# Kernel optimization log

Measured on AMD Instinct MI355X. Metric: run time of the kernel, lower is better.

The kernel has to match this reference:

```python
import jax, jax.numpy as jnp
import numpy as np

B, C, H, W = 8, 256, 64, 64
OUT, K = 256, 3
OG = 1
STRIDE, PAD, DIL = 1, 1, 1
K2 = K * K


def setup_inputs() -> dict:
    key = jax.random.key(0)
    ks = jax.random.split(key, 5)
    x = jax.random.normal(ks[0], (B, C, H, W), jnp.float32)
    # main deform-conv weight [out, in//groups, k, k]
    weight = jax.random.normal(ks[1], (OUT, C, K, K), jnp.float32) * (1.0 / np.sqrt(C * K2))
    bias = jax.random.normal(ks[2], (OUT,), jnp.float32) * 0.01
    # param_generator: 3x3 conv -> 3*OG*K*K channels (oh, ow, mask)
    pg_w = jax.random.normal(ks[3], (3 * OG * K2, C, 3, 3), jnp.float32) * 0.01
    pg_b = jax.random.normal(ks[4], (3 * OG * K2,), jnp.float32) * 0.01
    return {"x": x, "weight": weight, "bias": bias, "pg_w": pg_w, "pg_b": pg_b}


def _conv3x3(x, w, b):
    y = jax.lax.conv_general_dilated(
        x, w, (1, 1), [(1, 1), (1, 1)],
        dimension_numbers=("NCHW", "OIHW", "NCHW"))
    return y + b[None, :, None, None]


def _bilinear_gather(img, py, px):
    # img [B,C,H,W]; py,px [B,K2,Ho,Wo] -> [B,C,K2,Ho,Wo]
    # Zero padding outside the image (torchvision deform_conv2d semantics).
    Hh, Ww = img.shape[2], img.shape[3]
    y0 = jnp.floor(py)
    x0 = jnp.floor(px)
    dy = py - y0
    dx = px - x0
    imgf = img.reshape(img.shape[0], img.shape[1], Hh * Ww)
    out = jnp.zeros((img.shape[0], img.shape[1]) + py.shape[1:], img.dtype)
    corners = (
        (0, 0, (1 - dy) * (1 - dx)),
        (0, 1, (1 - dy) * dx),
        (1, 0, dy * (1 - dx)),
        (1, 1, dy * dx),
    )
    for oy, ox, wgt in corners:
        yy = y0 + oy
        xx = x0 + ox
        valid = (yy >= 0) & (yy < Hh) & (xx >= 0) & (xx < Ww)
        yi = jnp.clip(yy, 0, Hh - 1).astype(jnp.int32)
        xi = jnp.clip(xx, 0, Ww - 1).astype(jnp.int32)
        idx = yi * Ww + xi  # [B,K2,Ho,Wo]
        g = jax.vmap(lambda im, ix: jnp.take(im, ix.reshape(-1), axis=1))(imgf, idx)
        g = g.reshape(img.shape[0], img.shape[1], *idx.shape[1:])
        out = out + g * (wgt * valid)[:, None]
    return out


def _deform_conv2d(x, weight, bias, pg_w, pg_b):
    Bn = x.shape[0]
    Hi, Wi = x.shape[2], x.shape[3]
    Ho = (Hi + 2 * PAD - DIL * (K - 1) - 1) // STRIDE + 1
    Wo = (Wi + 2 * PAD - DIL * (K - 1) - 1) // STRIDE + 1
    params = _conv3x3(x, pg_w, pg_b)  # [B, 3*OG*K2, H, W]
    oh, ow, mask = jnp.split(params, 3, axis=1)
    offset = jnp.concatenate([oh, ow], axis=1)  # [B, 2*OG*K2, Ho, Wo]
    mask = jax.nn.sigmoid(mask)                  # [B, OG*K2, Ho, Wo]
    # torchvision layout: channel = ((og*K2 + k)*2 + {y,x})
    off = offset.reshape(Bn, OG, K2, 2, Ho, Wo)
    dy = off[:, :, :, 0].reshape(Bn, K2, Ho, Wo)  # OG == 1
    dx = off[:, :, :, 1].reshape(Bn, K2, Ho, Wo)
    hy = jnp.arange(Ho, dtype=x.dtype) * STRIDE - PAD
    wx = jnp.arange(Wo, dtype=x.dtype) * STRIDE - PAD
    ky, kx = jnp.meshgrid(jnp.arange(K), jnp.arange(K), indexing="ij")
    base_y = hy[None, :, None] + (ky.reshape(-1) * DIL).astype(x.dtype)[:, None, None]  # [K2,Ho,1]
    base_x = wx[None, None, :] + (kx.reshape(-1) * DIL).astype(x.dtype)[:, None, None]  # [K2,1,Wo]
    py = dy + base_y[None]  # [B,K2,Ho,Wo]
    px = dx + base_x[None]
    sampled = _bilinear_gather(x, py, px)          # [B,C,K2,Ho,Wo]
    sampled = sampled * mask[:, None]              # modulation (OG=1)
    out = jnp.einsum("bckhw,ock->bohw", sampled, weight.reshape(OUT, C, K2))
    return out + bias[None, :, None, None]


def reference(x, weight, bias, pg_w, pg_b):
    return _deform_conv2d(x, weight, bias, pg_w, pg_b)
```

## Files before the change

kernel.cpp:

```cpp
#include <hip/hip_runtime.h>
#include <math.h>

#define BQ   8
#define CIN  256
#define HH   64
#define WW   64
#define COUT 256
#define K2   9
#define PCH  27

#define PT     64
#define CCH    32
#define NCHUNK (CIN / CCH)
#define NSTEP  72
#define NSUB   24
#define SUBROW 104
#define PLANE  (HH * WW)

#define NXT    (BQ * HH * 4)
#define NPW    ((NSTEP * COUT * 4) / 256)
#define NPG    ((NSTEP * 32 * 4) / 256)
#define NPREP  (NXT + NPW + NPG)

typedef __attribute__((ext_vector_type(8))) short short8;
typedef __attribute__((ext_vector_type(4))) float f32x4;
typedef __attribute__((ext_vector_type(2))) float f32x2;

#define PIPE_BARRIER() do {                                   \
    asm volatile("s_waitcnt lgkmcnt(0)" ::: "memory");        \
    __builtin_amdgcn_s_barrier();                             \
    asm volatile("" ::: "memory");                            \
} while (0)

static __device__ __forceinline__ unsigned short f2bf(float f) {
    unsigned u = __builtin_bit_cast(unsigned, f);
    u += 0x7fff + ((u >> 16) & 1);
    return (unsigned short)(u >> 16);
}
static __device__ __forceinline__ f32x2 up2(unsigned u) {
    f32x2 r;
    r[0] = __builtin_bit_cast(float, u << 16);
    r[1] = __builtin_bit_cast(float, u & 0xffff0000u);
    return r;
}
static __device__ __forceinline__ unsigned cvtpk(float lo, float hi) {
    unsigned r;
    asm("v_cvt_pk_bf16_f32 %0, %1, %2" : "=v"(r) : "v"(lo), "v"(hi));
    return r;
}

__global__ __launch_bounds__(256) void k_prep(const float* __restrict__ x,
                                              unsigned short* __restrict__ xT,
                                              const float* __restrict__ w,
                                              unsigned short* __restrict__ wp,
                                              const float* __restrict__ pgw,
                                              unsigned short* __restrict__ wpg) {
    __shared__ float tile[64][65];
    int blk = blockIdx.x;

    if (blk < NXT) {
        int cc  = blk & 3;
        int y   = (blk >> 2) & 63;
        int b   = blk >> 8;
        int t   = threadIdx.x;
        int c0  = cc * 64;

        const float* xp = x + ((size_t)(b * CIN + c0) * HH + y) * WW;
#pragma unroll
        for (int r = 0; r < 16; ++r) {
            int cl = r * 4 + (t >> 6);
            int xx = t & 63;
            tile[cl][xx] = xp[(size_t)cl * PLANE + xx];
        }
        __syncthreads();
        unsigned short* op = xT + ((size_t)b * PLANE + (size_t)y * WW) * CIN + c0;
#pragma unroll
        for (int r = 0; r < 16; ++r) {
            int xx = r * 4 + (t >> 6);
            int cl = t & 63;
            op[(size_t)xx * CIN + cl] = f2bf(tile[cl][xx]);
        }
    } else if (blk < NXT + NPW) {
        int t = (blk - NXT) * 256 + threadIdx.x;
        int q = t & 3;
        int o = (t >> 2) & 255;
        int s = t >> 10;
        short8 sv;
#pragma unroll
        for (int j = 0; j < 8; ++j) {
            int pos   = s * 32 + q * 8 + j;
            int chunk = pos / (CCH * K2);
            int pl    = pos % (CCH * K2);
            int ktap  = pl >> 5;
            int c     = chunk * CCH + (pl & 31);
            sv[j] = (short)f2bf(w[(o * CIN + c) * K2 + ktap]);
        }
        *(short8*)(wp + (size_t)t * 8) = sv;
    } else {
        int t = (blk - NXT - NPW) * 256 + threadIdx.x;
        int q = t & 3;
        int o = (t >> 2) & 31;
        int s = t >> 7;
        short8 sv;
#pragma unroll
        for (int j = 0; j < 8; ++j) {
            int pos   = s * 32 + q * 8 + j;
            int chunk = pos / (CCH * K2);
            int pl    = pos % (CCH * K2);
            int ktap  = pl >> 5;
            int c     = chunk * CCH + (pl & 31);
            sv[j] = (o < PCH) ? (short)f2bf(pgw[(size_t)(o * CIN + c) * K2 + ktap]) : (short)0;
        }
        *(short8*)(wpg + (size_t)t * 8) = sv;
    }
}

__global__ __launch_bounds__(512, 2) void k_params(const unsigned short* __restrict__ xT,
                                                   const unsigned short* __restrict__ wpg,
                                                   const float* __restrict__ pgb,
                                                   float* __restrict__ pv) {
    __shared__ alignas(16) unsigned short s_rows[2][4][66][40];

    int blk = blockIdx.x;
    int swz = (blk & 7) * 32 + (blk >> 3);
    int b   = swz >> 5;
    int h0  = (swz & 31) * 2;
    int t   = threadIdx.x;

    int wv  = t >> 6;
    int lm  = t & 15;
    int lq  = (t >> 4) & 3;
    int ipg = wv >> 2;
    int seg = wv & 3;
    int ryb = seg >> 1;
    int pxb = (seg & 1) * 32;

    const unsigned short* xTb = xT + (size_t)b * PLANE * CIN;

    if (t < 64) {
        int buf = t >> 5;
        int ry  = (t >> 3) & 3;
        int col = ((t >> 2) & 1) * 65;
        int q   = t & 3;
        uint4 z = make_uint4(0, 0, 0, 0);
        *(uint4*)&s_rows[buf][ry][col][q * 8] = z;
    }
    __syncthreads();

    f32x4 acc0 = (f32x4){0.f, 0.f, 0.f, 0.f};
    f32x4 acc1 = (f32x4){0.f, 0.f, 0.f, 0.f};

    int pxm1 = t >> 3;
    int cgs  = (t & 7) * 4;

    uint2 R[4];
#pragma unroll
    for (int ry = 0; ry < 4; ++ry) {
        int y = h0 + ry - 1;
        R[ry] = make_uint2(0, 0);
        if ((unsigned)y < (unsigned)HH)
            R[ry] = *(const uint2*)(xTb + (size_t)(y * WW + pxm1) * CIN + cgs);
    }

    for (int ch = 0; ch < NCHUNK; ++ch) {
#pragma unroll
        for (int ry = 0; ry < 4; ++ry)
            *(uint2*)&s_rows[ch & 1][ry][pxm1 + 1][cgs] = R[ry];
        if (ch + 1 < NCHUNK) {
#pragma unroll
            for (int ry = 0; ry < 4; ++ry) {
                int y = h0 + ry - 1;
                R[ry] = make_uint2(0, 0);
                if ((unsigned)y < (unsigned)HH)
                    R[ry] = *(const uint2*)(xTb + (size_t)(y * WW + pxm1) * CIN
                                            + (ch + 1) * CCH + cgs);
            }
        }
        __syncthreads();
#pragma unroll
        for (int tap = 0; tap < K2; ++tap) {
            int ky = tap / 3, kx = tap % 3;
            short8 a  = *(const short8*)(wpg + (size_t)(ch * K2 + tap) * 32 * 32
                                         + (ipg * 16 + lm) * 32 + lq * 8);
            short8 bf0 = *(const short8*)&s_rows[ch & 1][ryb + ky][pxb +  0 + lm + kx][lq * 8];
            short8 bf1 = *(const short8*)&s_rows[ch & 1][ryb + ky][pxb + 16 + lm + kx][lq * 8];
            acc0 = __builtin_amdgcn_mfma_f32_16x16x32_bf16(a, bf0, acc0, 0, 0, 0);
            acc1 = __builtin_amdgcn_mfma_f32_16x16x32_bf16(a, bf1, acc1, 0, 0, 0);
        }
    }

    float* pvo = pv + ((size_t)(b * PCH) << 12) + (h0 + ryb) * WW;
#pragma unroll
    for (int rg = 0; rg < 4; ++rg) {
        int oc = ipg * 16 + lq * 4 + rg;
        if (oc < PCH) {
            float bb = pgb[oc];
            pvo[((size_t)oc << 12) + pxb +  0 + lm] = acc0[rg] + bb;
            pvo[((size_t)oc << 12) + pxb + 16 + lm] = acc1[rg] + bb;
        }
    }
}

__global__ __launch_bounds__(512, 4) void k_fused(const unsigned short* __restrict__ xT,
                                                  const unsigned short* __restrict__ wp,
                                                  const float* __restrict__ pv,
                                                  const float* __restrict__ bias,
                                                  float* __restrict__ out) {
    __shared__ alignas(16) unsigned short s_samp[2][PT][SUBROW];
    __shared__ float4 s_wgt4[K2][PT];
    __shared__ int4   s_off4[K2][PT];

    int blk = blockIdx.x;
    int swz = (blk & 7) * 64 + (blk >> 3);
    int b   = swz >> 6;
    int h   = swz & 63;
    int t   = threadIdx.x;

    int gp = t >> 3;
    int cg = t & 7;
    int wv = t >> 6;
    int lm = t & 15;
    int lq = (t >> 4) & 3;

    const char* xTb = (const char*)xT + (size_t)b * PLANE * CIN * 2;

    const float* pvb = pv + ((size_t)(b * PCH) << 12) + h * WW;
    for (int e = t; e < K2 * PT; e += 512) {
        int k = e >> 6;
        int p = e & 63;
        float dy = pvb[(size_t)(2 * k) << 12 | (unsigned)p];
        float dx = pvb[(size_t)(2 * k + 1) << 12 | (unsigned)p];
        float mz = pvb[(size_t)(18 + k) << 12 | (unsigned)p];
        float m  = 1.f / (1.f + expf(-mz));

        float py = dy + (float)(h - 1 + k / 3);
        float px = dx + (float)(p - 1 + k % 3);
        float y0f = floorf(py), x0f = floorf(px);
        float fy = py - y0f,    fx = px - x0f;
        int iy0 = (int)y0f, ix0 = (int)x0f;
        int iy1 = iy0 + 1,  ix1 = ix0 + 1;
        bool vy0 = (unsigned)iy0 < (unsigned)HH;
        bool vy1 = (unsigned)iy1 < (unsigned)HH;
        bool vx0 = (unsigned)ix0 < (unsigned)WW;
        bool vx1 = (unsigned)ix1 < (unsigned)WW;

        float w00 = (1.f - fy) * (1.f - fx) * m; if (!(vy0 && vx0)) w00 = 0.f;
        float w01 = (1.f - fy) * fx         * m; if (!(vy0 && vx1)) w01 = 0.f;
        float w10 = fy         * (1.f - fx) * m; if (!(vy1 && vx0)) w10 = 0.f;
        float w11 = fy         * fx         * m; if (!(vy1 && vx1)) w11 = 0.f;

        int cy0 = min(max(iy0, 0), HH - 1), cy1 = min(max(iy1, 0), HH - 1);
        int cx0 = min(max(ix0, 0), WW - 1), cx1 = min(max(ix1, 0), WW - 1);

        s_wgt4[k][p] = make_float4(w00, w01, w10, w11);
        s_off4[k][p] = make_int4((cy0 * WW + cx0) * 512, (cy0 * WW + cx1) * 512,
                                 (cy1 * WW + cx0) * 512, (cy1 * WW + cx1) * 512);
    }
    __syncthreads();

    int ow = wv * 32;
    f32x4 acc[2][4];
#pragma unroll
    for (int i = 0; i < 2; ++i)
#pragma unroll
        for (int j = 0; j < 4; ++j) acc[i][j] = (f32x4){0.f, 0.f, 0.f, 0.f};

    uint2 G[3][4];
    {
#pragma unroll
        for (int j = 0; j < 3; ++j) {
            int4 ob = s_off4[j][gp];
            G[j][0] = *(const uint2*)(xTb + ob.x + cg * 8);
            G[j][1] = *(const uint2*)(xTb + ob.y + cg * 8);
            G[j][2] = *(const uint2*)(xTb + ob.z + cg * 8);
            G[j][3] = *(const uint2*)(xTb + ob.w + cg * 8);
        }
#pragma unroll
        for (int j = 0; j < 3; ++j) {
            float4 gw = s_wgt4[j][gp];
            f32x2 v01 = gw.x * up2(G[j][0].x) + gw.y * up2(G[j][1].x)
                      + gw.z * up2(G[j][2].x) + gw.w * up2(G[j][3].x);
            f32x2 v23 = gw.x * up2(G[j][0].y) + gw.y * up2(G[j][1].y)
                      + gw.z * up2(G[j][2].y) + gw.w * up2(G[j][3].y);
            uint2 pk;
            pk.x = cvtpk(v01[0], v01[1]);
            pk.y = cvtpk(v23[0], v23[1]);
            *(uint2*)&s_samp[0][gp][j * 32 + cg * 4] = pk;
        }
#pragma unroll
        for (int j = 0; j < 3; ++j) {
            int4 ob = s_off4[3 + j][gp];
            G[j][0] = *(const uint2*)(xTb + ob.x + cg * 8);
            G[j][1] = *(const uint2*)(xTb + ob.y + cg * 8);
            G[j][2] = *(const uint2*)(xTb + ob.z + cg * 8);
            G[j][3] = *(const uint2*)(xTb + ob.w + cg * 8);
        }
        PIPE_BARRIER();
    }

    short8 a0c = *(const short8*)(wp + (ow +  0 + lm) * 32 + lq * 8);
    short8 a1c = *(const short8*)(wp + (ow + 16 + lm) * 32 + lq * 8);
    for (int sc = 0; sc < NSUB; ++sc) {
        bool doC = (sc + 1 < NSUB);
        bool doL = (sc + 2 < NSUB);
        int t1 = ((sc + 1) % 3) * 3;
        int t2 = ((sc + 2) % 3) * 3;
        int c2 = ((sc + 2) / 3) * (CCH * 2) + cg * 8;
        unsigned short (*__restrict__ bc)[SUBROW] = s_samp[sc & 1];
        unsigned short (*__restrict__ bn)[SUBROW] = s_samp[(sc + 1) & 1];
#pragma unroll
        for (int sl = 0; sl < 3; ++sl) {
            short8 b0 = *(const short8*)&bc[ 0 + lm][sl * 32 + lq * 8];
            short8 b1 = *(const short8*)&bc[16 + lm][sl * 32 + lq * 8];
            short8 b2 = *(const short8*)&bc[32 + lm][sl * 32 + lq * 8];
            short8 b3 = *(const short8*)&bc[48 + lm][sl * 32 + lq * 8];
            int r = sc * 3 + sl + 1;
            short8 a0n = a0c, a1n = a1c;
            if (r < NSTEP) {
                const unsigned short* wrn = wp + (size_t)r * COUT * 32;
                a0n = *(const short8*)(wrn + (ow +  0 + lm) * 32 + lq * 8);
                a1n = *(const short8*)(wrn + (ow + 16 + lm) * 32 + lq * 8);
            }
            if (doC) {
                float4 gw = s_wgt4[t1 + sl][gp];
                f32x2 v01 = gw.x * up2(G[sl][0].x) + gw.y * up2(G[sl][1].x)
                          + gw.z * up2(G[sl][2].x) + gw.w * up2(G[sl][3].x);
                f32x2 v23 = gw.x * up2(G[sl][0].y) + gw.y * up2(G[sl][1].y)
                          + gw.z * up2(G[sl][2].y) + gw.w * up2(G[sl][3].y);
                uint2 pk;
                pk.x = cvtpk(v01[0], v01[1]);
                pk.y = cvtpk(v23[0], v23[1]);
                *(uint2*)&bn[gp][sl * 32 + cg * 4] = pk;
            }
            if (doL) {
                int4 ob = s_off4[t2 + sl][gp];
                G[sl][0] = *(const uint2*)(xTb + ob.x + c2);
                G[sl][1] = *(const uint2*)(xTb + ob.y + c2);
                G[sl][2] = *(const uint2*)(xTb + ob.z + c2);
                G[sl][3] = *(const uint2*)(xTb + ob.w + c2);
            }
            acc[0][0] = __builtin_amdgcn_mfma_f32_16x16x32_bf16(a0c, b0, acc[0][0], 0, 0, 0);
            acc[0][1] = __builtin_amdgcn_mfma_f32_16x16x32_bf16(a0c, b1, acc[0][1], 0, 0, 0);
            acc[0][2] = __builtin_amdgcn_mfma_f32_16x16x32_bf16(a0c, b2, acc[0][2], 0, 0, 0);
            acc[0][3] = __builtin_amdgcn_mfma_f32_16x16x32_bf16(a0c, b3, acc[0][3], 0, 0, 0);
            acc[1][0] = __builtin_amdgcn_mfma_f32_16x16x32_bf16(a1c, b0, acc[1][0], 0, 0, 0);
            acc[1][1] = __builtin_amdgcn_mfma_f32_16x16x32_bf16(a1c, b1, acc[1][1], 0, 0, 0);
            acc[1][2] = __builtin_amdgcn_mfma_f32_16x16x32_bf16(a1c, b2, acc[1][2], 0, 0, 0);
            acc[1][3] = __builtin_amdgcn_mfma_f32_16x16x32_bf16(a1c, b3, acc[1][3], 0, 0, 0);
            a0c = a0n; a1c = a1n;
        }
        PIPE_BARRIER();
    }

    float* op = out + ((size_t)b * COUT) * PLANE + h * WW;
#pragma unroll
    for (int i = 0; i < 2; ++i) {
        int o0 = ow + i * 16 + lq * 4;
        f32x4 bv = *(const f32x4*)(bias + o0);
#pragma unroll
        for (int rg = 0; rg < 4; ++rg) {
#pragma unroll
            for (int j = 0; j < 4; ++j)
                op[(size_t)(o0 + rg) * PLANE + j * 16 + lm] = acc[i][j][rg] + bv[rg];
        }
    }
}

extern "C" void kernel_launch(void* const* d_in, const int* in_sizes, int n_in,
                              void* d_out, int out_size, void* d_ws, size_t ws_size,
                              hipStream_t stream) {
    const float* x    = (const float*)d_in[0];
    const float* wgt  = (const float*)d_in[1];
    const float* bias = (const float*)d_in[2];
    const float* pgw  = (const float*)d_in[3];
    const float* pgb  = (const float*)d_in[4];
    float* out = (float*)d_out;

    const size_t WPK_B = (size_t)NSTEP * COUT * 32 * 2;
    const size_t WPG_B = (size_t)NSTEP * 32 * 32 * 2;
    const size_t XT_B  = (size_t)BQ * PLANE * CIN * 2;
    unsigned short* wpk = (unsigned short*)d_ws;
    unsigned short* wpg = (unsigned short*)((char*)d_ws + WPK_B);
    unsigned short* xT  = (unsigned short*)((char*)d_ws + WPK_B + WPG_B);
    float*          pv  = (float*)((char*)d_ws + WPK_B + WPG_B + XT_B);

    k_prep  <<<NPREP, 256, 0, stream>>>(x, xT, wgt, wpk, pgw, wpg);
    k_params<<<BQ * HH / 2, 512, 0, stream>>>(xT, wpg, pgb, pv);
    k_fused <<<BQ * HH, 512, 0, stream>>>(xT, wpk, pv, bias, out);
}
```

Measured before the change: 104.3 us.

## Split fused deform-conv block into producer and consumer wave groups

```diff
diff --git a/kernel.cpp b/kernel.cpp
--- a/kernel.cpp
+++ b/kernel.cpp
@@ -216,8 +216,6 @@
     int h   = swz & 63;
     int t   = threadIdx.x;
 
-    int gp = t >> 3;
-    int cg = t & 7;
     int wv = t >> 6;
     int lm = t & 15;
     int lq = (t >> 4) & 3;
@@ -258,22 +256,28 @@
     }
     __syncthreads();
 
-    int ow = wv * 32;
-    f32x4 acc[2][4];
-#pragma unroll
-    for (int i = 0; i < 2; ++i)
+    bool producer = (wv < 4);
+    int gp = t >> 2;
+    int cq = t & 3;
+    int ow = (wv - 4) * 64;
+
+    f32x4 acc[4][4];
+#pragma unroll
+    for (int i = 0; i < 4; ++i)
 #pragma unroll
         for (int j = 0; j < 4; ++j) acc[i][j] = (f32x4){0.f, 0.f, 0.f, 0.f};
 
-    uint2 G[3][4];
-    {
+    uint4 G[3][4];
+    short8 aC[4], aN[4];
+
+    if (producer) {
 #pragma unroll
         for (int j = 0; j < 3; ++j) {
             int4 ob = s_off4[j][gp];
-            G[j][0] = *(const uint2*)(xTb + ob.x + cg * 8);
-            G[j][1] = *(const uint2*)(xTb + ob.y + cg * 8);
-            G[j][2] = *(const uint2*)(xTb + ob.z + cg * 8);
-            G[j][3] = *(const uint2*)(xTb + ob.w + cg * 8);
+            G[j][0] = *(const uint4*)(xTb + ob.x + cq * 16);
+            G[j][1] = *(const uint4*)(xTb + ob.y + cq * 16);
+            G[j][2] = *(const uint4*)(xTb + ob.z + cq * 16);
+            G[j][3] = *(const uint4*)(xTb + ob.w + cq * 16);
         }
 #pragma unroll
         for (int j = 0; j < 3; ++j) {
@@ -282,86 +286,119 @@
                       + gw.z * up2(G[j][2].x) + gw.w * up2(G[j][3].x);
             f32x2 v23 = gw.x * up2(G[j][0].y) + gw.y * up2(G[j][1].y)
                       + gw.z * up2(G[j][2].y) + gw.w * up2(G[j][3].y);
-            uint2 pk;
+            f32x2 v45 = gw.x * up2(G[j][0].z) + gw.y * up2(G[j][1].z)
+                      + gw.z * up2(G[j][2].z) + gw.w * up2(G[j][3].z);
+            f32x2 v67 = gw.x * up2(G[j][0].w) + gw.y * up2(G[j][1].w)
+                      + gw.z * up2(G[j][2].w) + gw.w * up2(G[j][3].w);
+            uint4 pk;
             pk.x = cvtpk(v01[0], v01[1]);
             pk.y = cvtpk(v23[0], v23[1]);
-            *(uint2*)&s_samp[0][gp][j * 32 + cg * 4] = pk;
+            pk.z = cvtpk(v45[0], v45[1]);
+            pk.w = cvtpk(v67[0], v67[1]);
+            *(uint4*)&s_samp[0][gp][j * 32 + cq * 8] = pk;
         }
 #pragma unroll
         for (int j = 0; j < 3; ++j) {
             int4 ob = s_off4[3 + j][gp];
-            G[j][0] = *(const uint2*)(xTb + ob.x + cg * 8);
-            G[j][1] = *(const uint2*)(xTb + ob.y + cg * 8);
-            G[j][2] = *(const uint2*)(xTb + ob.z + cg * 8);
-            G[j][3] = *(const uint2*)(xTb + ob.w + cg * 8);
-        }
-        PIPE_BARRIER();
-    }
-
-    short8 a0c = *(const short8*)(wp + (ow +  0 + lm) * 32 + lq * 8);
-    short8 a1c = *(const short8*)(wp + (ow + 16 + lm) * 32 + lq * 8);
+            G[j][0] = *(const uint4*)(xTb + ob.x + cq * 16);
+            G[j][1] = *(const uint4*)(xTb + ob.y + cq * 16);
+            G[j][2] = *(const uint4*)(xTb + ob.z + cq * 16);
+            G[j][3] = *(const uint4*)(xTb + ob.w + cq * 16);
+        }
+    } else {
+#pragma unroll
+        for (int i = 0; i < 4; ++i)
+            aC[i] = *(const short8*)(wp + (ow + i * 16 + lm) * 32 + lq * 8);
+    }
+    PIPE_BARRIER();
+
     for (int sc = 0; sc < NSUB; ++sc) {
-        bool doC = (sc + 1 < NSUB);
-        bool doL = (sc + 2 < NSUB);
-        int t1 = ((sc + 1) % 3) * 3;
-        int t2 = ((sc + 2) % 3) * 3;
-        int c2 = ((sc + 2) / 3) * (CCH * 2) + cg * 8;
         unsigned short (*__restrict__ bc)[SUBROW] = s_samp[sc & 1];
         unsigned short (*__restrict__ bn)[SUBROW] = s_samp[(sc + 1) & 1];
-#pragma unroll
-        for (int sl = 0; sl < 3; ++sl) {
-            short8 b0 = *(const short8*)&bc[ 0 + lm][sl * 32 + lq * 8];
-            short8 b1 = *(const short8*)&bc[16 + lm][sl * 32 + lq * 8];
-            short8 b2 = *(const short8*)&bc[32 + lm][sl * 32 + lq * 8];
-            short8 b3 = *(const short8*)&bc[48 + lm][sl * 32 + lq * 8];
-            int r = sc * 3 + sl + 1;
-            short8 a0n = a0c, a1n = a1c;
-            if (r < NSTEP) {
-                const unsigned short* wrn = wp + (size_t)r * COUT * 32;
-                a0n = *(const short8*)(wrn + (ow +  0 + lm) * 32 + lq * 8);
-                a1n = *(const short8*)(wrn + (ow + 16 + lm) * 32 + lq * 8);
+        if (producer) {
+            bool doC = (sc + 1 < NSUB);
+            bool doL = (sc + 2 < NSUB);
+            int t1 = ((sc + 1) % 3) * 3;
+            int t2 = ((sc + 2) % 3) * 3;
+            int c2 = ((sc + 2) / 3) * (CCH * 2) + cq * 16;
+#pragma unroll
+            for (int sl = 0; sl < 3; ++sl) {
+                if (doC) {
+                    float4 gw = s_wgt4[t1 + sl][gp];
+                    f32x2 v01 = gw.x * up2(G[sl][0].x) + gw.y * up2(G[sl][1].x)
+                              + gw.z * up2(G[sl][2].x) + gw.w * up2(G[sl][3].x);
+                    f32x2 v23 = gw.x * up2(G[sl][0].y) + gw.y * up2(G[sl][1].y)
+                              + gw.z * up2(G[sl][2].y) + gw.w * up2(G[sl][3].y);
+                    f32x2 v45 = gw.x * up2(G[sl][0].z) + gw.y * up2(G[sl][1].z)
+                              + gw.z * up2(G[sl][2].z) + gw.w * up2(G[sl][3].z);
+                    f32x2 v67 = gw.x * up2(G[sl][0].w) + gw.y * up2(G[sl][1].w)
+                              + gw.z * up2(G[sl][2].w) + gw.w * up2(G[sl][3].w);
+                    uint4 pk;
+                    pk.x = cvtpk(v01[0], v01[1]);
+                    pk.y = cvtpk(v23[0], v23[1]);
+                    pk.z = cvtpk(v45[0], v45[1]);
+                    pk.w = cvtpk(v67[0], v67[1]);
+                    *(uint4*)&bn[gp][sl * 32 + cq * 8] = pk;
+                }
+                if (doL) {
+                    int4 ob = s_off4[t2 + sl][gp];
+                    G[sl][0] = *(const uint4*)(xTb + ob.x + c2);
+                    G[sl][1] = *(const uint4*)(xTb + ob.y + c2);
+                    G[sl][2] = *(const uint4*)(xTb + ob.z + c2);
+                    G[sl][3] = *(const uint4*)(xTb + ob.w + c2);
+                }
             }
-            if (doC) {
-                float4 gw = s_wgt4[t1 + sl][gp];
-                f32x2 v01 = gw.x * up2(G[sl][0].x) + gw.y * up2(G[sl][1].x)
-                          + gw.z * up2(G[sl][2].x) + gw.w * up2(G[sl][3].x);
-                f32x2 v23 = gw.x * up2(G[sl][0].y) + gw.y * up2(G[sl][1].y)
-                          + gw.z * up2(G[sl][2].y) + gw.w * up2(G[sl][3].y);
-                uint2 pk;
-                pk.x = cvtpk(v01[0], v01[1]);
-                pk.y = cvtpk(v23[0], v23[1]);
-                *(uint2*)&bn[gp][sl * 32 + cg * 4] = pk;
+        } else {
+#pragma unroll
+            for (int sl = 0; sl < 3; ++sl) {
+                short8 b0 = *(const short8*)&bc[ 0 + lm][sl * 32 + lq * 8];
+                short8 b1 = *(const short8*)&bc[16 + lm][sl * 32 + lq * 8];
+                short8 b2 = *(const short8*)&bc[32 + lm][sl * 32 + lq * 8];
+                short8 b3 = *(const short8*)&bc[48 + lm][sl * 32 + lq * 8];
+                int r = sc * 3 + sl + 1;
+#pragma unroll
+                for (int i = 0; i < 4; ++i) aN[i] = aC[i];
+                if (r < NSTEP) {
+                    const unsigned short* wrn = wp + (size_t)r * COUT * 32;
+#pragma unroll
+                    for (int i = 0; i < 4; ++i)
+                        aN[i] = *(const short8*)(wrn + (ow + i * 16 + lm) * 32 + lq * 8);
+                }
+                acc[0][0] = __builtin_amdgcn_mfma_f32_16x16x32_bf16(aC[0], b0, acc[0][0], 0, 0, 0);
+                acc[0][1] = __builtin_amdgcn_mfma_f32_16x16x32_bf16(aC[0], b1, acc[0][1], 0, 0, 0);
+                acc[0][2] = __builtin_amdgcn_mfma_f32_16x16x32_bf16(aC[0], b2, acc[0][2], 0, 0, 0);
+                acc[0][3] = __builtin_amdgcn_mfma_f32_16x16x32_bf16(aC[0], b3, acc[0][3], 0, 0, 0);
+                acc[1][0] = __builtin_amdgcn_mfma_f32_16x16x32_bf16(aC[1], b0, acc[1][0], 0, 0, 0);
+                acc[1][1] = __builtin_amdgcn_mfma_f32_16x16x32_bf16(aC[1], b1, acc[1][1], 0, 0, 0);
+                acc[1][2] = __builtin_amdgcn_mfma_f32_16x16x32_bf16(aC[1], b2, acc[1][2], 0, 0, 0);
+                acc[1][3] = __builtin_amdgcn_mfma_f32_16x16x32_bf16(aC[1], b3, acc[1][3], 0, 0, 0);
+                acc[2][0] = __builtin_amdgcn_mfma_f32_16x16x32_bf16(aC[2], b0, acc[2][0], 0, 0, 0);
+                acc[2][1] = __builtin_amdgcn_mfma_f32_16x16x32_bf16(aC[2], b1, acc[2][1], 0, 0, 0);
+                acc[2][2] = __builtin_amdgcn_mfma_f32_16x16x32_bf16(aC[2], b2, acc[2][2], 0, 0, 0);
+                acc[2][3] = __builtin_amdgcn_mfma_f32_16x16x32_bf16(aC[2], b3, acc[2][3], 0, 0, 0);
+                acc[3][0] = __builtin_amdgcn_mfma_f32_16x16x32_bf16(aC[3], b0, acc[3][0], 0, 0, 0);
+                acc[3][1] = __builtin_amdgcn_mfma_f32_16x16x32_bf16(aC[3], b1, acc[3][1], 0, 0, 0);
+                acc[3][2] = __builtin_amdgcn_mfma_f32_16x16x32_bf16(aC[3], b2, acc[3][2], 0, 0, 0);
+                acc[3][3] = __builtin_amdgcn_mfma_f32_16x16x32_bf16(aC[3], b3, acc[3][3], 0, 0, 0);
+#pragma unroll
+                for (int i = 0; i < 4; ++i) aC[i] = aN[i];
             }
-            if (doL) {
-                int4 ob = s_off4[t2 + sl][gp];
-                G[sl][0] = *(const uint2*)(xTb + ob.x + c2);
-                G[sl][1] = *(const uint2*)(xTb + ob.y + c2);
-                G[sl][2] = *(const uint2*)(xTb + ob.z + c2);
-                G[sl][3] = *(const uint2*)(xTb + ob.w + c2);
+        }
+        PIPE_BARRIER();
+    }
+
+    if (!producer) {
+        float* op = out + ((size_t)b * COUT) * PLANE + h * WW;
+#pragma unroll
+        for (int i = 0; i < 4; ++i) {
+            int o0 = ow + i * 16 + lq * 4;
+            f32x4 bv = *(const f32x4*)(bias + o0);
+#pragma unroll
+            for (int rg = 0; rg < 4; ++rg) {
+#pragma unroll
+                for (int j = 0; j < 4; ++j)
+                    op[(size_t)(o0 + rg) * PLANE + j * 16 + lm] = acc[i][j][rg] + bv[rg];
             }
-            acc[0][0] = __builtin_amdgcn_mfma_f32_16x16x32_bf16(a0c, b0, acc[0][0], 0, 0, 0);
-            acc[0][1] = __builtin_amdgcn_mfma_f32_16x16x32_bf16(a0c, b1, acc[0][1], 0, 0, 0);
-            acc[0][2] = __builtin_amdgcn_mfma_f32_16x16x32_bf16(a0c, b2, acc[0][2], 0, 0, 0);
-            acc[0][3] = __builtin_amdgcn_mfma_f32_16x16x32_bf16(a0c, b3, acc[0][3], 0, 0, 0);
-            acc[1][0] = __builtin_amdgcn_mfma_f32_16x16x32_bf16(a1c, b0, acc[1][0], 0, 0, 0);
-            acc[1][1] = __builtin_amdgcn_mfma_f32_16x16x32_bf16(a1c, b1, acc[1][1], 0, 0, 0);
-            acc[1][2] = __builtin_amdgcn_mfma_f32_16x16x32_bf16(a1c, b2, acc[1][2], 0, 0, 0);
-            acc[1][3] = __builtin_amdgcn_mfma_f32_16x16x32_bf16(a1c, b3, acc[1][3], 0, 0, 0);
-            a0c = a0n; a1c = a1n;
-        }
-        PIPE_BARRIER();
-    }
-
-    float* op = out + ((size_t)b * COUT) * PLANE + h * WW;
-#pragma unroll
-    for (int i = 0; i < 2; ++i) {
-        int o0 = ow + i * 16 + lq * 4;
-        f32x4 bv = *(const f32x4*)(bias + o0);
-#pragma unroll
-        for (int rg = 0; rg < 4; ++rg) {
-#pragma unroll
-            for (int j = 0; j < 4; ++j)
-                op[(size_t)(o0 + rg) * PLANE + j * 16 + lm] = acc[i][j][rg] + bv[rg];
         }
     }
 }
```

New measurement: 267.1 us. +156.1%, slower.
